# Performance work log

Measured on AMD Instinct MI355X. Metric: run time of the kernel, lower is better.

The kernel has to match this reference:

```python
import jax, jax.numpy as jnp
import numpy as np
from jax import lax

SIGMA = 1.0          # block_elemnts.combined_sigma
BN_EPS = 1e-5


def setup_inputs() -> dict:
    key = jax.random.key(0)
    k1, k2, k3, k4 = jax.random.split(key, 4)
    B, N, T, C_in, C_out = 8, 1024, 8, 64, 64
    return {
        "points": jax.random.normal(k1, (B, N, 3), dtype=jnp.float32),
        "translations": jax.random.normal(k2, (B, T, 3), dtype=jnp.float32),
        "functions": jax.random.normal(k3, (B, N, C_in), dtype=jnp.float32),
        "k_tensor": jax.random.normal(k4, (C_out, C_in, T), dtype=jnp.float32)
            * np.sqrt(2.0 / (C_in + C_out)),  # xavier_normal_
        "gamma": jnp.ones((C_out,), dtype=jnp.float32),
        "beta": jnp.zeros((C_out,), dtype=jnp.float32),
    }


def reference(points, translations, functions, k_tensor, gamma, beta):
    denom = 2.0 * SIGMA ** 2
    # pairwise squared distances [B,N,N]
    sq = jnp.sum(points * points, axis=-1)                      # [B,N]
    dist = sq[:, :, None] + sq[:, None, :] \
        - 2.0 * jnp.einsum('bnd,bmd->bnm', points, points)      # [B,N,N]
    # interpolation matrix = Gaussian kernel of distances
    interp_rowsum = jnp.sum(jnp.exp(-dist / denom), axis=2, keepdims=True)  # [B,N,1]
    w = functions / interp_rowsum                               # [B,N,Cin]
    # b_tensor[t] = w @ k_tensor[:,:,t]^T  -> [T,B,N,Cout]
    b = jnp.einsum('bnc,oct->tbno', w, k_tensor)
    ptd = jnp.einsum('bnd,btd->tbn', points, translations)      # [T,B,N]
    tsq = jnp.sum(translations * translations, axis=2).T        # [T,B]

    B_, N_, O_ = b.shape[1], b.shape[2], b.shape[3]

    def step(acc, inputs):
        b_t, ptd_t, tsq_t = inputs                              # [B,N,O],[B,N],[B]
        dot = -2.0 * ptd_t                                      # [B,N]
        # exponent = -||p_i - p_j - t||^2 / (2*sigma^2), always <= 0
        q = jnp.exp(-(dist + dot[:, :, None] - dot[:, None, :]
                      + tsq_t[:, None, None]) / denom)          # [B,N,N]
        return acc + jnp.einsum('bnm,bmo->bno', q, b_t), None

    out, _ = lax.scan(step, jnp.zeros((B_, N_, O_), dtype=b.dtype),
                      (b, ptd, tsq))                            # [B,N,O]

    # BatchNorm1d in training mode over (B,N) per channel, then ReLU
    mean = jnp.mean(out, axis=(0, 1))
    var = jnp.var(out, axis=(0, 1))
    xn = (out - mean) * lax.rsqrt(var + BN_EPS) * gamma + beta
    return jax.nn.relu(xn)                                      # [B,N,Cout]
```

## Files before the change

### kernel.cpp

```cpp
#include <hip/hip_runtime.h>
#include <hip/hip_bf16.h>
#include <cstdint>
#include <cstddef>

#define BN_EPS 1e-5f

typedef float f32x4_t __attribute__((ext_vector_type(4)));
typedef __bf16 bf16x8_t __attribute__((ext_vector_type(8)));

__device__ __forceinline__ unsigned short f2bf(float f) {
    __hip_bfloat16 h = __float2bfloat16(f);
    return __builtin_bit_cast(unsigned short, h);
}
__device__ __forceinline__ float bf2f(unsigned short u) {
    unsigned int v = ((unsigned int)u) << 16;
    return __builtin_bit_cast(float, v);
}

__device__ __forceinline__ void gld_lds16(void* lds, const void* gp) {
#if __has_builtin(__builtin_amdgcn_global_load_lds)
    __builtin_amdgcn_global_load_lds(
        (const __attribute__((address_space(1))) unsigned int*)gp,
        (__attribute__((address_space(3))) unsigned int*)lds, 16, 0, 0);
#else
    *(uint4*)lds = *(const uint4*)gp;
#endif
}


union SmemGP {
    struct {
        float praw[3072];
        float px[1024], py[1024], pz[1024], hq[1024];
        float part[16][128];
        float p2[16][32];
    } g;
    struct {
        unsigned short Asm[128 * 72];
        unsigned short Bsm[128 * 72];
        float sfacl[256];
    } p;
};

__global__ __launch_bounds__(256) void k_gp(const float* __restrict__ points,
                                            const float* __restrict__ trans,
                                            const float* __restrict__ funcs,
                                            const float* __restrict__ ktens,
                                            float* __restrict__ rowsum,
                                            unsigned short* __restrict__ bmatT,
                                            float* __restrict__ escale,
                                            float* __restrict__ bns) {
    __shared__ SmemGP smu;
    const int tid = threadIdx.x;

    if (blockIdx.x >= 512) {
        const int bk = blockIdx.x - 512;
        const int b  = bk & 7;
        const int mt = (bk >> 3) & 7;
        const int ct = bk >> 6;
        const int m0 = mt * 128;

        unsigned short* Asm = smu.p.Asm;
        unsigned short* Bsm = smu.p.Bsm;
        float* sfacl = smu.p.sfacl;

        if (blockIdx.x == 512 && tid < 128) bns[tid] = 0.f;

        const int wave = tid >> 6, lane = tid & 63;
        const int wr = wave >> 1, wc = wave & 1;
        const int fr = lane & 15, quad = lane >> 4;

        {
            const int tloc = tid >> 7, m = tid & 127;
            const int t = ct * 2 + tloc;
            const float tx = trans[b * 24 + t * 3], ty = trans[b * 24 + t * 3 + 1],
                        tz = trans[b * 24 + t * 3 + 2];
            const float* pp = &points[(size_t)(b * 1024 + m0 + m) * 3];
            const float ptd = pp[0] * tx + pp[1] * ty + pp[2] * tz;
            const float tsq = tx * tx + ty * ty + tz * tz;
            sfacl[tloc * 128 + m] = __expf(-ptd - 0.5f * tsq);
            escale[(size_t)(b * 8 + t) * 1024 + m0 + m] = __expf(ptd);
        }
        #pragma unroll
        for (int rep = 0; rep < 2; ++rep) {
            const int m = rep * 64 + (tid >> 2);
            const int c16 = (tid & 3) * 16;
            const float* fp = &funcs[((size_t)(b * 1024) + m0 + m) * 64 + c16];
            float4 f0 = *(const float4*)fp, f1 = *(const float4*)(fp + 4);
            float4 f2 = *(const float4*)(fp + 8), f3 = *(const float4*)(fp + 12);
            uint4 p0, p1;
            p0.x = f2bf(f0.x) | ((unsigned)f2bf(f0.y) << 16);
            p0.y = f2bf(f0.z) | ((unsigned)f2bf(f0.w) << 16);
            p0.z = f2bf(f1.x) | ((unsigned)f2bf(f1.y) << 16);
            p0.w = f2bf(f1.z) | ((unsigned)f2bf(f1.w) << 16);
            p1.x = f2bf(f2.x) | ((unsigned)f2bf(f2.y) << 16);
            p1.y = f2bf(f2.z) | ((unsigned)f2bf(f2.w) << 16);
            p1.z = f2bf(f3.x) | ((unsigned)f2bf(f3.y) << 16);
            p1.w = f2bf(f3.z) | ((unsigned)f2bf(f3.w) << 16);
            *(uint4*)&Asm[m * 72 + c16] = p0;
            *(uint4*)&Asm[m * 72 + c16 + 8] = p1;
        }
        #pragma unroll
        for (int rep = 0; rep < 4; ++rep) {
            const int col = rep * 32 + (tid >> 3);
            const int c8  = (tid & 7) * 8;
            const int g   = ct * 128 + col;
            const int t   = g >> 6, o = g & 63;
            const float* kt = &ktens[(size_t)(o * 64 + c8) * 8 + t];
            unsigned short us[8];
            #pragma unroll
            for (int q = 0; q < 8; ++q) us[q] = f2bf(kt[q * 8]);
            uint4 v;
            v.x = us[0] | ((unsigned)us[1] << 16);
            v.y = us[2] | ((unsigned)us[3] << 16);
            v.z = us[4] | ((unsigned)us[5] << 16);
            v.w = us[6] | ((unsigned)us[7] << 16);
            *(uint4*)&Bsm[col * 72 + c8] = v;
        }
        __syncthreads();

        f32x4_t acc[4][4];
        #pragma unroll
        for (int i = 0; i < 4; ++i)
            #pragma unroll
            for (int j = 0; j < 4; ++j) acc[i][j] = f32x4_t{0.f, 0.f, 0.f, 0.f};

        #pragma unroll
        for (int s = 0; s < 2; ++s) {
            uint4 afr[4], bfr[4];
            #pragma unroll
            for (int i = 0; i < 4; ++i)
                afr[i] = *(const uint4*)&Asm[(wr * 64 + i * 16 + fr) * 72 + s * 32 + quad * 8];
            #pragma unroll
            for (int j = 0; j < 4; ++j)
                bfr[j] = *(const uint4*)&Bsm[(wc * 64 + j * 16 + fr) * 72 + s * 32 + quad * 8];
            #pragma unroll
            for (int i = 0; i < 4; ++i)
                #pragma unroll
                for (int j = 0; j < 4; ++j)
                    acc[i][j] = __builtin_amdgcn_mfma_f32_16x16x32_bf16(
                        __builtin_bit_cast(bf16x8_t, afr[i]),
                        __builtin_bit_cast(bf16x8_t, bfr[j]),
                        acc[i][j], 0, 0, 0);
        }

        #pragma unroll
        for (int i = 0; i < 4; ++i) {
            #pragma unroll
            for (int j = 0; j < 4; ++j) {
                const int colg = ct * 128 + wc * 64 + j * 16 + fr;
                ushort4 pk;
                const int mb = wr * 64 + i * 16 + quad * 4;
                pk.x = f2bf(acc[i][j][0] * sfacl[wc * 128 + mb + 0]);
                pk.y = f2bf(acc[i][j][1] * sfacl[wc * 128 + mb + 1]);
                pk.z = f2bf(acc[i][j][2] * sfacl[wc * 128 + mb + 2]);
                pk.w = f2bf(acc[i][j][3] * sfacl[wc * 128 + mb + 3]);
                *(ushort4*)&bmatT[(size_t)(b * 512 + colg) * 1024 + m0 + mb] = pk;
            }
        }
        return;
    }

    float* praw = smu.g.praw;
    float* px = smu.g.px; float* py = smu.g.py;
    float* pz = smu.g.pz; float* hq = smu.g.hq;
    float (*part)[128] = smu.g.part;
    float (*p2)[32] = smu.g.p2;

    const int b  = blockIdx.x & 7;
    const int n0 = (blockIdx.x >> 3) * 16;

    for (int i = tid; i < 3072; i += 256) praw[i] = points[b * 3072 + i];
    __syncthreads();
    for (int n = tid; n < 1024; n += 256) {
        float x = praw[n * 3], y = praw[n * 3 + 1], z = praw[n * 3 + 2];
        px[n] = x; py[n] = y; pz[n] = z;
        hq[n] = -0.5f * (x * x + y * y + z * z);
    }
    __syncthreads();

    const int rhalf = tid >> 7;
    const int c0 = (tid & 127) * 8;
    float vx[8], vy[8], vz[8], vh[8];
    *(float4*)&vx[0] = *(const float4*)&px[c0];
    *(float4*)&vx[4] = *(const float4*)&px[c0 + 4];
    *(float4*)&vy[0] = *(const float4*)&py[c0];
    *(float4*)&vy[4] = *(const float4*)&py[c0 + 4];
    *(float4*)&vz[0] = *(const float4*)&pz[c0];
    *(float4*)&vz[4] = *(const float4*)&pz[c0 + 4];
    *(float4*)&vh[0] = *(const float4*)&hq[c0];
    *(float4*)&vh[4] = *(const float4*)&hq[c0 + 4];

    #pragma unroll
    for (int u = 0; u < 8; ++u) {
        const int rl = u * 2 + rhalf;
        const int row = n0 + rl;
        const float rx = px[row], ry = py[row], rz = pz[row], hr = hq[row];
        float ssum = 0.f;
        #pragma unroll
        for (int j = 0; j < 8; ++j)
            ssum += __expf(hr + vh[j] + rx * vx[j] + ry * vy[j] + rz * vz[j]);
        part[rl][tid & 127] = ssum;
    }
    __syncthreads();
    #pragma unroll
    for (int rep = 0; rep < 2; ++rep) {
        const int row = rep * 8 + (tid >> 5), c4l = (tid & 31) * 4;
        float4 p = *(const float4*)&part[row][c4l];
        p2[row][tid & 31] = p.x + p.y + p.z + p.w;
    }
    __syncthreads();
    if (tid < 16) {
        float s = 0.f;
        #pragma unroll
        for (int q = 0; q < 8; ++q) {
            float4 v = *(const float4*)&p2[tid][q * 4];
            s += v.x + v.y + v.z + v.w;
        }
        rowsum[b * 1024 + n0 + tid] = s;
    }
}

__global__ __launch_bounds__(256, 2) void k_gemm(const float* __restrict__ points,
                                                 const unsigned short* __restrict__ bmatT,
                                                 const float* __restrict__ escale,
                                                 const float* __restrict__ rowsum,
                                                 unsigned short* __restrict__ He2) {
    __shared__ unsigned short Bs[8192];
    __shared__ float escT[1024];
    __shared__ float4 mp[256];

    const int b  = blockIdx.x & 7;
    const int rt = (blockIdx.x >> 3) & 7;
    const int z  = blockIdx.x >> 6;
    const int ogp = z & 1;
    const int kh  = z >> 1;
    const int n0 = rt * 128;
    const int kb = kh * 256;

    const int tid  = threadIdx.x;
    const int wave = tid >> 6, lane = tid & 63;

    {
        const int t = tid >> 5, r4 = (tid & 31) * 4;
        *(float4*)&escT[t * 128 + r4] =
            *(const float4*)&escale[(size_t)(b * 8 + t) * 1024 + n0 + r4];
    }
    {
        const float* pp = &points[(size_t)(b * 1024 + kb + tid) * 3];
        const float x = pp[0], y = pp[1], zz = pp[2];
        const float rs = rowsum[b * 1024 + kb + tid];
        mp[tid] = make_float4(x, y, zz,
                              -0.5f * (x * x + y * y + zz * zz) - __logf(rs));
    }

    const unsigned short* gB = bmatT + (size_t)(b * 512 + ogp * 32) * 1024 + kb;

    const int r16 = lane >> 2;
    const int kq  = lane & 3;
    const int gsw = kq ^ (r16 & 3);

    const int fr = lane & 15;
    const int quad = lane >> 4;
    const int swoff = (quad ^ (fr & 3)) << 4;
    const int row_base = wave * 32;

    float rx0, ry0, rz0, rh0, rx1, ry1, rz1, rh1;
    {
        const float* p0 = &points[(size_t)(b * 1024 + n0 + row_base + fr) * 3];
        rx0 = p0[0]; ry0 = p0[1]; rz0 = p0[2];
        rh0 = -0.5f * (rx0 * rx0 + ry0 * ry0 + rz0 * rz0);
        const float* p1 = &points[(size_t)(b * 1024 + n0 + row_base + 16 + fr) * 3];
        rx1 = p1[0]; ry1 = p1[1]; rz1 = p1[2];
        rh1 = -0.5f * (rx1 * rx1 + ry1 * ry1 + rz1 * rz1);
    }

    f32x4_t acc[2][16];
    #pragma unroll
    for (int i = 0; i < 2; ++i)
        #pragma unroll
        for (int j = 0; j < 16; ++j) acc[i][j] = f32x4_t{0.f, 0.f, 0.f, 0.f};

    for (int kk = 0; kk < 8; ++kk) {
        const int k0 = kk * 32;
        __syncthreads();
        #pragma unroll
        for (int i = 0; i < 4; ++i) {
            const int seg = wave * 4 + i;
            const int t = seg >> 1, oh = (seg & 1) * 16;
            gld_lds16((char*)Bs + seg * 1024 + lane * 16,
                      gB + (size_t)(t * 64 + oh + r16) * 1024 + k0 + gsw * 8);
        }
        uint4 afr0, afr1;
        {
            unsigned short u0[8], u1[8];
            const int mbase = k0 + quad * 8;
            #pragma unroll
            for (int j = 0; j < 8; ++j) {
                const float4 m4 = mp[mbase + j];
                const float e0 = __expf(rh0 + m4.w + rx0 * m4.x + ry0 * m4.y + rz0 * m4.z);
                const float e1 = __expf(rh1 + m4.w + rx1 * m4.x + ry1 * m4.y + rz1 * m4.z);
                u0[j] = f2bf(e0);
                u1[j] = f2bf(e1);
            }
            afr0.x = u0[0] | ((unsigned)u0[1] << 16);
            afr0.y = u0[2] | ((unsigned)u0[3] << 16);
            afr0.z = u0[4] | ((unsigned)u0[5] << 16);
            afr0.w = u0[6] | ((unsigned)u0[7] << 16);
            afr1.x = u1[0] | ((unsigned)u1[1] << 16);
            afr1.y = u1[2] | ((unsigned)u1[3] << 16);
            afr1.z = u1[4] | ((unsigned)u1[5] << 16);
            afr1.w = u1[6] | ((unsigned)u1[7] << 16);
        }
        __syncthreads();
        #pragma unroll
        for (int j = 0; j < 16; ++j) {
            uint4 bfr = *(const uint4*)((const char*)Bs + (j * 16 + fr) * 64 + swoff);
            acc[0][j] = __builtin_amdgcn_mfma_f32_16x16x32_bf16(
                __builtin_bit_cast(bf16x8_t, afr0),
                __builtin_bit_cast(bf16x8_t, bfr), acc[0][j], 0, 0, 0);
            acc[1][j] = __builtin_amdgcn_mfma_f32_16x16x32_bf16(
                __builtin_bit_cast(bf16x8_t, afr1),
                __builtin_bit_cast(bf16x8_t, bfr), acc[1][j], 0, 0, 0);
        }
    }

    const int oo = lane & 15;
    unsigned short* dst = He2 + (size_t)kh * 524288
                              + (size_t)(b * 1024 + n0) * 64 + ogp * 32;
    #pragma unroll
    for (int i = 0; i < 2; ++i) {
        #pragma unroll
        for (int r = 0; r < 4; ++r) {
            const int row = row_base + i * 16 + quad * 4 + r;
            float s0 = 0.f, s1 = 0.f;
            #pragma unroll
            for (int t = 0; t < 8; ++t) {
                const float e = escT[t * 128 + row];
                s0 += e * acc[i][2 * t][r];
                s1 += e * acc[i][2 * t + 1][r];
            }
            dst[(size_t)row * 64 + oo] = f2bf(s0);
            dst[(size_t)row * 64 + 16 + oo] = f2bf(s1);
        }
    }
}

__global__ __launch_bounds__(256) void k_fin(const unsigned short* __restrict__ He2,
                                             float* __restrict__ out,
                                             float* __restrict__ bns) {
    __shared__ float s1[16][64], s2[16][64];
    const int tid = threadIdx.x;
    const int vb = ((blockIdx.x & 7) << 5) | (blockIdx.x >> 3);
    float a0 = 0.f, a1 = 0.f, a2 = 0.f, a3 = 0.f;
    float q0 = 0.f, q1 = 0.f, q2 = 0.f, q3 = 0.f;
    #pragma unroll
    for (int it = 0; it < 2; ++it) {
        const size_t idx = (size_t)vb * 512 + it * 256 + tid;
        float4 s = make_float4(0.f, 0.f, 0.f, 0.f);
        #pragma unroll
        for (int p = 0; p < 4; ++p) {
            ushort4 u = *(const ushort4*)(He2 + (size_t)p * 524288 + idx * 4);
            s.x += bf2f(u.x); s.y += bf2f(u.y); s.z += bf2f(u.z); s.w += bf2f(u.w);
        }
        ((float4*)out)[idx] = s;
        a0 += s.x; a1 += s.y; a2 += s.z; a3 += s.w;
        q0 += s.x * s.x; q1 += s.y * s.y; q2 += s.z * s.z; q3 += s.w * s.w;
    }
    const int g = tid >> 4, o4 = (tid & 15) * 4;
    *(float4*)&s1[g][o4] = make_float4(a0, a1, a2, a3);
    *(float4*)&s2[g][o4] = make_float4(q0, q1, q2, q3);
    __syncthreads();
    if (tid < 64) {
        float sa = 0.f, sb = 0.f;
        #pragma unroll
        for (int r = 0; r < 16; ++r) { sa += s1[r][tid]; sb += s2[r][tid]; }
        atomicAdd(&bns[tid], sa);
        atomicAdd(&bns[64 + tid], sb);
    }
}

__global__ __launch_bounds__(256) void k_bn(float* __restrict__ out,
                                            const float* __restrict__ bns,
                                            const float* __restrict__ gamma,
                                            const float* __restrict__ beta) {
    const int vb = ((blockIdx.x & 7) << 6) | (blockIdx.x >> 3);
    const int i = vb * 256 + threadIdx.x;
    const int o4 = (i & 15) * 4;
    float4 x = ((float4*)out)[i];
    const float4 s  = *(const float4*)&bns[o4];
    const float4 s2 = *(const float4*)&bns[64 + o4];
    const float4 gm = *(const float4*)&gamma[o4];
    const float4 bt = *(const float4*)&beta[o4];
    const float invn = 1.f / 8192.f;
    float m, v, w;
    m = s.x * invn; v = s2.x * invn - m * m; w = __frsqrt_rn(v + BN_EPS) * gm.x;
    x.x = fmaxf((x.x - m) * w + bt.x, 0.f);
    m = s.y * invn; v = s2.y * invn - m * m; w = __frsqrt_rn(v + BN_EPS) * gm.y;
    x.y = fmaxf((x.y - m) * w + bt.y, 0.f);
    m = s.z * invn; v = s2.z * invn - m * m; w = __frsqrt_rn(v + BN_EPS) * gm.z;
    x.z = fmaxf((x.z - m) * w + bt.z, 0.f);
    m = s.w * invn; v = s2.w * invn - m * m; w = __frsqrt_rn(v + BN_EPS) * gm.w;
    x.w = fmaxf((x.w - m) * w + bt.w, 0.f);
    ((float4*)out)[i] = x;
}

extern "C" void kernel_launch(void* const* d_in, const int* in_sizes, int n_in,
                              void* d_out, int out_size, void* d_ws, size_t ws_size,
                              hipStream_t stream) {
    const float* points = (const float*)d_in[0];
    const float* trans  = (const float*)d_in[1];
    const float* funcs  = (const float*)d_in[2];
    const float* ktens  = (const float*)d_in[3];
    const float* gamma  = (const float*)d_in[4];
    const float* beta   = (const float*)d_in[5];
    float* out = (float*)d_out;

    float* ws      = (float*)d_ws;
    float* escale  = ws;
    float* bns     = escale + 65536;
    float* rowsum  = bns + 128;
    unsigned short* He2   = (unsigned short*)(rowsum + 8192);
    unsigned short* bmatT = He2 + 2097152;

    k_gp<<<768, 256, 0, stream>>>(points, trans, funcs, ktens,
                                  rowsum, bmatT, escale, bns);
    k_gemm<<<512, 256, 0, stream>>>(points, bmatT, escale, rowsum, He2);
    k_fin<<<256, 256, 0, stream>>>(He2, out, bns);
    k_bn<<<512, 256, 0, stream>>>(out, bns, gamma, beta);
}
```

Baseline: 103.1 us.

## Triple-buffer B tiles in k_gemm with async prefetch and exp2-based Gaussians

Triple-buffers the B operand in LDS inside k_gemm, issuing global-to-LDS loads for the next k-slice while the current slice's Gaussian weights are computed. Explicit vmcnt waits and one barrier per iteration replace the two __syncthreads per iteration. The exponent is prescaled by log2(e) so that raw exp2 instructions replace __expf, bf16 packing now converts pairs with the packed intrinsic, and the epilogue reads escale with vector loads. This trades more LDS per block and hand-written waitcnt logic, which could be wrong if the count of outstanding loads differs, for less stalling on memory and fewer ALU ops.

Measured after the change: 102.6 us, median of 2. About the same (-0.5%).

```diff
diff --git a/kernel.cpp b/kernel.cpp
--- a/kernel.cpp
+++ b/kernel.cpp
@@ -2,8 +2,10 @@
 #include <hip/hip_bf16.h>
 #include <cstdint>
 #include <cstddef>
+#include <cstring>
 
 #define BN_EPS 1e-5f
+#define L2E 1.4426950408889634f
 
 typedef float f32x4_t __attribute__((ext_vector_type(4)));
 typedef __bf16 bf16x8_t __attribute__((ext_vector_type(8)));
@@ -15,6 +17,12 @@
 __device__ __forceinline__ float bf2f(unsigned short u) {
     unsigned int v = ((unsigned int)u) << 16;
     return __builtin_bit_cast(float, v);
+}
+__device__ __forceinline__ unsigned int pkbf(float a, float b) {
+    __hip_bfloat162 h = __float22bfloat162_rn(make_float2(a, b));
+    unsigned int r;
+    __builtin_memcpy(&r, &h, 4);
+    return r;
 }
 
 __device__ __forceinline__ void gld_lds16(void* lds, const void* gp) {
@@ -89,14 +97,10 @@
             float4 f0 = *(const float4*)fp, f1 = *(const float4*)(fp + 4);
             float4 f2 = *(const float4*)(fp + 8), f3 = *(const float4*)(fp + 12);
             uint4 p0, p1;
-            p0.x = f2bf(f0.x) | ((unsigned)f2bf(f0.y) << 16);
-            p0.y = f2bf(f0.z) | ((unsigned)f2bf(f0.w) << 16);
-            p0.z = f2bf(f1.x) | ((unsigned)f2bf(f1.y) << 16);
-            p0.w = f2bf(f1.z) | ((unsigned)f2bf(f1.w) << 16);
-            p1.x = f2bf(f2.x) | ((unsigned)f2bf(f2.y) << 16);
-            p1.y = f2bf(f2.z) | ((unsigned)f2bf(f2.w) << 16);
-            p1.z = f2bf(f3.x) | ((unsigned)f2bf(f3.y) << 16);
-            p1.w = f2bf(f3.z) | ((unsigned)f2bf(f3.w) << 16);
+            p0.x = pkbf(f0.x, f0.y); p0.y = pkbf(f0.z, f0.w);
+            p0.z = pkbf(f1.x, f1.y); p0.w = pkbf(f1.z, f1.w);
+            p1.x = pkbf(f2.x, f2.y); p1.y = pkbf(f2.z, f2.w);
+            p1.z = pkbf(f3.x, f3.y); p1.w = pkbf(f3.z, f3.w);
             *(uint4*)&Asm[m * 72 + c16] = p0;
             *(uint4*)&Asm[m * 72 + c16 + 8] = p1;
         }
@@ -107,14 +111,11 @@
             const int g   = ct * 128 + col;
             const int t   = g >> 6, o = g & 63;
             const float* kt = &ktens[(size_t)(o * 64 + c8) * 8 + t];
-            unsigned short us[8];
-            #pragma unroll
-            for (int q = 0; q < 8; ++q) us[q] = f2bf(kt[q * 8]);
             uint4 v;
-            v.x = us[0] | ((unsigned)us[1] << 16);
-            v.y = us[2] | ((unsigned)us[3] << 16);
-            v.z = us[4] | ((unsigned)us[5] << 16);
-            v.w = us[6] | ((unsigned)us[7] << 16);
+            v.x = pkbf(kt[0], kt[8]);
+            v.y = pkbf(kt[16], kt[24]);
+            v.z = pkbf(kt[32], kt[40]);
+            v.w = pkbf(kt[48], kt[56]);
             *(uint4*)&Bsm[col * 72 + c8] = v;
         }
         __syncthreads();
@@ -149,13 +150,13 @@
             #pragma unroll
             for (int j = 0; j < 4; ++j) {
                 const int colg = ct * 128 + wc * 64 + j * 16 + fr;
-                ushort4 pk;
                 const int mb = wr * 64 + i * 16 + quad * 4;
-                pk.x = f2bf(acc[i][j][0] * sfacl[wc * 128 + mb + 0]);
-                pk.y = f2bf(acc[i][j][1] * sfacl[wc * 128 + mb + 1]);
-                pk.z = f2bf(acc[i][j][2] * sfacl[wc * 128 + mb + 2]);
-                pk.w = f2bf(acc[i][j][3] * sfacl[wc * 128 + mb + 3]);
-                *(ushort4*)&bmatT[(size_t)(b * 512 + colg) * 1024 + m0 + mb] = pk;
+                uint2 pk;
+                pk.x = pkbf(acc[i][j][0] * sfacl[wc * 128 + mb + 0],
+                            acc[i][j][1] * sfacl[wc * 128 + mb + 1]);
+                pk.y = pkbf(acc[i][j][2] * sfacl[wc * 128 + mb + 2],
+                            acc[i][j][3] * sfacl[wc * 128 + mb + 3]);
+                *(uint2*)&bmatT[(size_t)(b * 512 + colg) * 1024 + m0 + mb] = pk;
             }
         }
         return;
@@ -175,7 +176,7 @@
     for (int n = tid; n < 1024; n += 256) {
         float x = praw[n * 3], y = praw[n * 3 + 1], z = praw[n * 3 + 2];
         px[n] = x; py[n] = y; pz[n] = z;
-        hq[n] = -0.5f * (x * x + y * y + z * z);
+        hq[n] = -0.5f * L2E * (x * x + y * y + z * z);
     }
     __syncthreads();
 
@@ -195,11 +196,13 @@
     for (int u = 0; u < 8; ++u) {
         const int rl = u * 2 + rhalf;
         const int row = n0 + rl;
-        const float rx = px[row], ry = py[row], rz = pz[row], hr = hq[row];
+        const float rx = L2E * px[row], ry = L2E * py[row], rz = L2E * pz[row];
+        const float hr = hq[row];
         float ssum = 0.f;
         #pragma unroll
         for (int j = 0; j < 8; ++j)
-            ssum += __expf(hr + vh[j] + rx * vx[j] + ry * vy[j] + rz * vz[j]);
+            ssum += __builtin_amdgcn_exp2f(hr + vh[j] + rx * vx[j]
+                                           + ry * vy[j] + rz * vz[j]);
         part[rl][tid & 127] = ssum;
     }
     __syncthreads();
@@ -226,7 +229,7 @@
                                                  const float* __restrict__ escale,
                                                  const float* __restrict__ rowsum,
                                                  unsigned short* __restrict__ He2) {
-    __shared__ unsigned short Bs[8192];
+    __shared__ unsigned short Bs[3][8192];
     __shared__ float escT[1024];
     __shared__ float4 mp[256];
 
@@ -241,19 +244,6 @@
     const int tid  = threadIdx.x;
     const int wave = tid >> 6, lane = tid & 63;
 
-    {
-        const int t = tid >> 5, r4 = (tid & 31) * 4;
-        *(float4*)&escT[t * 128 + r4] =
-            *(const float4*)&escale[(size_t)(b * 8 + t) * 1024 + n0 + r4];
-    }
-    {
-        const float* pp = &points[(size_t)(b * 1024 + kb + tid) * 3];
-        const float x = pp[0], y = pp[1], zz = pp[2];
-        const float rs = rowsum[b * 1024 + kb + tid];
-        mp[tid] = make_float4(x, y, zz,
-                              -0.5f * (x * x + y * y + zz * zz) - __logf(rs));
-    }
-
     const unsigned short* gB = bmatT + (size_t)(b * 512 + ogp * 32) * 1024 + kb;
 
     const int r16 = lane >> 2;
@@ -268,12 +258,35 @@
     float rx0, ry0, rz0, rh0, rx1, ry1, rz1, rh1;
     {
         const float* p0 = &points[(size_t)(b * 1024 + n0 + row_base + fr) * 3];
-        rx0 = p0[0]; ry0 = p0[1]; rz0 = p0[2];
-        rh0 = -0.5f * (rx0 * rx0 + ry0 * ry0 + rz0 * rz0);
+        const float x0 = p0[0], y0 = p0[1], z0 = p0[2];
+        rh0 = -0.5f * L2E * (x0 * x0 + y0 * y0 + z0 * z0);
+        rx0 = L2E * x0; ry0 = L2E * y0; rz0 = L2E * z0;
         const float* p1 = &points[(size_t)(b * 1024 + n0 + row_base + 16 + fr) * 3];
-        rx1 = p1[0]; ry1 = p1[1]; rz1 = p1[2];
-        rh1 = -0.5f * (rx1 * rx1 + ry1 * ry1 + rz1 * rz1);
-    }
+        const float x1 = p1[0], y1 = p1[1], z1 = p1[2];
+        rh1 = -0.5f * L2E * (x1 * x1 + y1 * y1 + z1 * z1);
+        rx1 = L2E * x1; ry1 = L2E * y1; rz1 = L2E * z1;
+    }
+    {
+        const int t = tid >> 5, r4 = (tid & 31) * 4;
+        float4 ev = *(const float4*)&escale[(size_t)(b * 8 + t) * 1024 + n0 + r4];
+        const float* pp = &points[(size_t)(b * 1024 + kb + tid) * 3];
+        const float x = pp[0], y = pp[1], zz = pp[2];
+        const float rs = rowsum[b * 1024 + kb + tid];
+        *(float4*)&escT[t * 128 + r4] = ev;
+        mp[tid] = make_float4(x, y, zz,
+                              -0.5f * L2E * (x * x + y * y + zz * zz)
+                              - __builtin_amdgcn_logf(rs));
+    }
+    __builtin_amdgcn_sched_barrier(0);
+    #pragma unroll
+    for (int i = 0; i < 4; ++i) {
+        const int seg = wave * 4 + i;
+        const int tt = seg >> 1, oh = (seg & 1) * 16;
+        gld_lds16((char*)Bs[0] + seg * 1024 + lane * 16,
+                  gB + (size_t)(tt * 64 + oh + r16) * 1024 + gsw * 8);
+    }
+    asm volatile("s_waitcnt lgkmcnt(0)" ::: "memory");
+    __builtin_amdgcn_s_barrier();
 
     f32x4_t acc[2][16];
     #pragma unroll
@@ -281,41 +294,43 @@
         #pragma unroll
         for (int j = 0; j < 16; ++j) acc[i][j] = f32x4_t{0.f, 0.f, 0.f, 0.f};
 
+    #pragma unroll
     for (int kk = 0; kk < 8; ++kk) {
-        const int k0 = kk * 32;
-        __syncthreads();
-        #pragma unroll
-        for (int i = 0; i < 4; ++i) {
-            const int seg = wave * 4 + i;
-            const int t = seg >> 1, oh = (seg & 1) * 16;
-            gld_lds16((char*)Bs + seg * 1024 + lane * 16,
-                      gB + (size_t)(t * 64 + oh + r16) * 1024 + k0 + gsw * 8);
+        const int cur = kk % 3;
+        if (kk < 7) {
+            const int nxt = (kk + 1) % 3;
+            const int k0n = (kk + 1) * 32;
+            #pragma unroll
+            for (int i = 0; i < 4; ++i) {
+                const int seg = wave * 4 + i;
+                const int tt = seg >> 1, oh = (seg & 1) * 16;
+                gld_lds16((char*)Bs[nxt] + seg * 1024 + lane * 16,
+                          gB + (size_t)(tt * 64 + oh + r16) * 1024 + k0n + gsw * 8);
+            }
         }
         uint4 afr0, afr1;
         {
-            unsigned short u0[8], u1[8];
-            const int mbase = k0 + quad * 8;
+            const int mbase = kk * 32 + quad * 8;
+            float e0[8], e1[8];
             #pragma unroll
             for (int j = 0; j < 8; ++j) {
                 const float4 m4 = mp[mbase + j];
-                const float e0 = __expf(rh0 + m4.w + rx0 * m4.x + ry0 * m4.y + rz0 * m4.z);
-                const float e1 = __expf(rh1 + m4.w + rx1 * m4.x + ry1 * m4.y + rz1 * m4.z);
-                u0[j] = f2bf(e0);
-                u1[j] = f2bf(e1);
+                e0[j] = __builtin_amdgcn_exp2f(rh0 + m4.w + rx0 * m4.x
+                                               + ry0 * m4.y + rz0 * m4.z);
+                e1[j] = __builtin_amdgcn_exp2f(rh1 + m4.w + rx1 * m4.x
+                                               + ry1 * m4.y + rz1 * m4.z);
             }
-            afr0.x = u0[0] | ((unsigned)u0[1] << 16);
-            afr0.y = u0[2] | ((unsigned)u0[3] << 16);
-            afr0.z = u0[4] | ((unsigned)u0[5] << 16);
-            afr0.w = u0[6] | ((unsigned)u0[7] << 16);
-            afr1.x = u1[0] | ((unsigned)u1[1] << 16);
-            afr1.y = u1[2] | ((unsigned)u1[3] << 16);
-            afr1.z = u1[4] | ((unsigned)u1[5] << 16);
-            afr1.w = u1[6] | ((unsigned)u1[7] << 16);
-        }
-        __syncthreads();
+            afr0.x = pkbf(e0[0], e0[1]); afr0.y = pkbf(e0[2], e0[3]);
+            afr0.z = pkbf(e0[4], e0[5]); afr0.w = pkbf(e0[6], e0[7]);
+            afr1.x = pkbf(e1[0], e1[1]); afr1.y = pkbf(e1[2], e1[3]);
+            afr1.z = pkbf(e1[4], e1[5]); afr1.w = pkbf(e1[6], e1[7]);
+        }
+        if (kk < 7) asm volatile("s_waitcnt vmcnt(4)" ::: "memory");
+        else        asm volatile("s_waitcnt vmcnt(0)" ::: "memory");
+        __builtin_amdgcn_s_barrier();
         #pragma unroll
         for (int j = 0; j < 16; ++j) {
-            uint4 bfr = *(const uint4*)((const char*)Bs + (j * 16 + fr) * 64 + swoff);
+            uint4 bfr = *(const uint4*)((const char*)Bs[cur] + (j * 16 + fr) * 64 + swoff);
             acc[0][j] = __builtin_amdgcn_mfma_f32_16x16x32_bf16(
                 __builtin_bit_cast(bf16x8_t, afr0),
                 __builtin_bit_cast(bf16x8_t, bfr), acc[0][j], 0, 0, 0);
@@ -330,18 +345,20 @@
                               + (size_t)(b * 1024 + n0) * 64 + ogp * 32;
     #pragma unroll
     for (int i = 0; i < 2; ++i) {
+        const int rb = row_base + i * 16 + quad * 4;
+        float s0[4] = {0.f, 0.f, 0.f, 0.f}, s1[4] = {0.f, 0.f, 0.f, 0.f};
+        #pragma unroll
+        for (int t = 0; t < 8; ++t) {
+            const float4 ev = *(const float4*)&escT[t * 128 + rb];
+            s0[0] += ev.x * acc[i][2 * t][0]; s1[0] += ev.x * acc[i][2 * t + 1][0];
+            s0[1] += ev.y * acc[i][2 * t][1]; s1[1] += ev.y * acc[i][2 * t + 1][1];
+            s0[2] += ev.z * acc[i][2 * t][2]; s1[2] += ev.z * acc[i][2 * t + 1][2];
+            s0[3] += ev.w * acc[i][2 * t][3]; s1[3] += ev.w * acc[i][2 * t + 1][3];
+        }
         #pragma unroll
         for (int r = 0; r < 4; ++r) {
-            const int row = row_base + i * 16 + quad * 4 + r;
-            float s0 = 0.f, s1 = 0.f;
-            #pragma unroll
-            for (int t = 0; t < 8; ++t) {
-                const float e = escT[t * 128 + row];
-                s0 += e * acc[i][2 * t][r];
-                s1 += e * acc[i][2 * t + 1][r];
-            }
-            dst[(size_t)row * 64 + oo] = f2bf(s0);
-            dst[(size_t)row * 64 + 16 + oo] = f2bf(s1);
+            dst[(size_t)(rb + r) * 64 + oo] = f2bf(s0[r]);
+            dst[(size_t)(rb + r) * 64 + 16 + oo] = f2bf(s1[r]);
         }
     }
 }
```
